# Kernel tuning notes

Hardware: AMD Instinct MI355X
Metric: run time of the kernel (lower is better)

The kernel has to match this reference:

```python
import jax, jax.numpy as jnp
import numpy as np

N = 50000       # population nodes
E = 1_600_000   # edges per edge type
F_IN = 2000     # flattened individual-graph embedding (100*20)
D = 20          # hidden channels per TransformerConv head (heads=1)
NEG_SLOPE = 0.01
BN_EPS = 1e-5


def setup_inputs() -> dict:
    key = jax.random.key(0)
    ks = jax.random.split(key, 24)
    features = jax.random.normal(ks[0], (N, F_IN), jnp.float32)
    same_index = jax.random.randint(ks[1], (2, E), 0, N, dtype=jnp.int64)
    diff_index = jax.random.randint(ks[2], (2, E), 0, N, dtype=jnp.int64)
    s0 = 1.0 / np.sqrt(F_IN)
    s1 = 1.0 / np.sqrt(D)
    # layer 0 conv params, stacked over the 2 edge types (same, diff)
    W0q = jax.random.normal(ks[3], (2, F_IN, D), jnp.float32) * s0
    W0k = jax.random.normal(ks[4], (2, F_IN, D), jnp.float32) * s0
    W0v = jax.random.normal(ks[5], (2, F_IN, D), jnp.float32) * s0
    W0s = jax.random.normal(ks[6], (2, F_IN, D), jnp.float32) * s0
    b0q = jnp.zeros((2, D)); b0k = jnp.zeros((2, D))
    b0v = jnp.zeros((2, D)); b0s = jnp.zeros((2, D))
    # layers 1..3 conv params: [layer, edge_type, D, D]
    Wq = jax.random.normal(ks[7], (3, 2, D, D), jnp.float32) * s1
    Wk = jax.random.normal(ks[8], (3, 2, D, D), jnp.float32) * s1
    Wv = jax.random.normal(ks[9], (3, 2, D, D), jnp.float32) * s1
    Ws = jax.random.normal(ks[10], (3, 2, D, D), jnp.float32) * s1
    bq = jnp.zeros((3, 2, D)); bk = jnp.zeros((3, 2, D))
    bv = jnp.zeros((3, 2, D)); bs = jnp.zeros((3, 2, D))
    w1 = jnp.full((4,), 0.8, jnp.float32)
    w2 = jnp.full((4,), 0.2, jnp.float32)
    bn_gamma = jnp.ones((4, D), jnp.float32)
    bn_beta = jnp.zeros((4, D), jnp.float32)
    Wout = jax.random.normal(ks[11], (4 * D, 2), jnp.float32) / np.sqrt(4 * D)
    bout = jnp.zeros((2,), jnp.float32)
    return dict(features=features, same_index=same_index, diff_index=diff_index,
                W0q=W0q, b0q=b0q, W0k=W0k, b0k=b0k, W0v=W0v, b0v=b0v, W0s=W0s, b0s=b0s,
                Wq=Wq, bq=bq, Wk=Wk, bk=bk, Wv=Wv, bv=bv, Ws=Ws, bs=bs,
                w1=w1, w2=w2, bn_gamma=bn_gamma, bn_beta=bn_beta, Wout=Wout, bout=bout)


def _tconv(x, edge_index, Wq, bq, Wk, bk, Wv, bv, Ws, bs):
    """PyG TransformerConv, heads=1, concat=True, root_weight=True, no edge_attr."""
    src, dst = edge_index[0], edge_index[1]
    q = x @ Wq + bq   # [N, D]
    k = x @ Wk + bk
    v = x @ Wv + bv
    logits = jnp.einsum('ed,ed->e', q[dst], k[src]) / jnp.sqrt(jnp.float32(D))  # [E]
    m = jax.ops.segment_max(logits, dst, num_segments=N)
    m = jnp.where(jnp.isfinite(m), m, jnp.float32(0.0))  # nodes with no in-edges
    e = jnp.exp(logits - m[dst])
    z = jax.ops.segment_sum(e, dst, num_segments=N)
    alpha = e / (z[dst] + 1e-16)  # PyG softmax epsilon
    agg = jax.ops.segment_sum(alpha[:, None] * v[src], dst, num_segments=N)  # [N, D]
    return agg + x @ Ws + bs  # skip (root) connection


def _bn(x, gamma, beta):
    mu = x.mean(axis=0)
    var = x.var(axis=0)
    return (x - mu) * jax.lax.rsqrt(var + BN_EPS) * gamma + beta


def reference(features, same_index, diff_index,
              W0q, b0q, W0k, b0k, W0v, b0v, W0s, b0s,
              Wq, bq, Wk, bk, Wv, bv, Ws, bs,
              w1, w2, bn_gamma, bn_beta, Wout, bout):
    x = features
    fcs = []
    for l in range(4):
        if l == 0:
            p_same = (W0q[0], b0q[0], W0k[0], b0k[0], W0v[0], b0v[0], W0s[0], b0s[0])
            p_diff = (W0q[1], b0q[1], W0k[1], b0k[1], W0v[1], b0v[1], W0s[1], b0s[1])
        else:
            i = l - 1
            p_same = (Wq[i, 0], bq[i, 0], Wk[i, 0], bk[i, 0], Wv[i, 0], bv[i, 0], Ws[i, 0], bs[i, 0])
            p_diff = (Wq[i, 1], bq[i, 1], Wk[i, 1], bk[i, 1], Wv[i, 1], bv[i, 1], Ws[i, 1], bs[i, 1])
        x1 = _tconv(x, same_index, *p_same)
        x2 = _tconv(x, diff_index, *p_diff)
        t = w1[l] + w2[l]
        x = (w1[l] / t) * x1 + (w2[l] / t) * x2
        x = _bn(x, bn_gamma[l], bn_beta[l])
        x = jax.nn.leaky_relu(x, NEG_SLOPE)
        fcs.append(x)
    fc = jnp.concatenate(fcs, axis=-1)  # [N, 80]
    return fc @ Wout + bout  # [N, 2]
```

## Files before the change

### kernel.cpp

```cpp
#include <hip/hip_runtime.h>
#include <math.h>

#define N_NODES 50000
#define E_EDGES 1600000
#define F_IN    2000
#define D       20
#define NCOL    160
#define KPAD    2016

#define INV_SQRT_D 0.22360679774997896f

typedef __bf16 bf16x8 __attribute__((ext_vector_type(8)));
typedef __bf16 bf16x4 __attribute__((ext_vector_type(4)));
typedef float  f32x4  __attribute__((ext_vector_type(4)));

__global__ void pack_kernel(
    const float* __restrict__ W0q, const float* __restrict__ W0k,
    const float* __restrict__ W0v, const float* __restrict__ W0s,
    const float* __restrict__ b0q, const float* __restrict__ b0k,
    const float* __restrict__ b0v, const float* __restrict__ b0s,
    const float* __restrict__ Wq,  const float* __restrict__ Wk,
    const float* __restrict__ Wv,  const float* __restrict__ Ws_,
    const float* __restrict__ bq,  const float* __restrict__ bk,
    const float* __restrict__ bv,  const float* __restrict__ bs_,
    __bf16* __restrict__ B0, float* __restrict__ bias0,
    float* __restrict__ WL, float* __restrict__ biasL,
    float* __restrict__ bn, int* __restrict__ deg)
{
  long idx = (long)blockIdx.x * blockDim.x + threadIdx.x;
  if (idx < (long)NCOL*KPAD) {
    int col = (int)(idx / KPAD), k = (int)(idx % KPAD);
    int et = col / 80, r = col % 80, mat = r / 20, d = r % 20;
    const float* w = (mat==0)?W0q:(mat==1)?W0s:(mat==2)?W0k:W0v;
    float v = (k < F_IN) ? w[((size_t)et*F_IN + k)*D + d] : 0.f;
    B0[idx] = (__bf16)v;
    return;
  }
  idx -= (long)NCOL*KPAD;
  if (idx < 160) {
    int col = (int)idx;
    int et = col / 80, r = col % 80, mat = r / 20, d = r % 20;
    const float* b = (mat==0)?b0q:(mat==1)?b0s:(mat==2)?b0k:b0v;
    bias0[col] = b[et*D + d];
    return;
  }
  idx -= 160;
  if (idx < 9600) {
    int l = (int)(idx / 3200), rem = (int)(idx % 3200);
    int k = rem / NCOL, col = rem % NCOL;
    int et = col / 80, r = col % 80, mat = r / 20, d = r % 20;
    const float* w = (mat==0)?Wq:(mat==1)?Ws_:(mat==2)?Wk:Wv;
    WL[idx] = w[(((size_t)l*2 + et)*D + k)*D + d];
    return;
  }
  idx -= 9600;
  if (idx < 480) {
    int l = (int)(idx / NCOL), col = (int)(idx % NCOL);
    int et = col / 80, r = col % 80, mat = r / 20, d = r % 20;
    const float* b = (mat==0)?bq:(mat==1)?bs_:(mat==2)?bk:bv;
    biasL[idx] = b[(l*2 + et)*D + d];
    return;
  }
  idx -= 480;
  if (idx < 320) { bn[idx] = 0.f; return; }
  idx -= 320;
  if (idx < 2*N_NODES) { deg[idx] = 0; return; }
}

__global__ void hist_kernel(const int* __restrict__ same, const int* __restrict__ diff,
                            int* __restrict__ deg)
{
  long i = (long)blockIdx.x * blockDim.x + threadIdx.x;
  if (i >= 2L*E_EDGES) return;
  int et = (i >= E_EDGES) ? 1 : 0;
  long e = i - (long)et*E_EDGES;
  const int* ix = et ? diff : same;
  int dst = ix[E_EDGES + e];
  atomicAdd(&deg[(size_t)et*N_NODES + dst], 1);
}

__global__ void scan_kernel(const int* __restrict__ deg,
                            int* __restrict__ rowptr0, int* __restrict__ rowptr1,
                            int* __restrict__ next0, int* __restrict__ next1)
{
  const int et = blockIdx.x;
  const int* dg = deg + (size_t)et*N_NODES;
  int* rp = et ? rowptr1 : rowptr0;
  int* np = et ? next1 : next0;
  __shared__ int part[1024];
  const int t = threadIdx.x;
  const int per = (N_NODES + 1023) / 1024;
  const int b = t * per;
  const int e = (b + per < N_NODES) ? (b + per) : N_NODES;
  int s = 0;
  for (int i = b; i < e; i++) s += dg[i];
  part[t] = s;
  __syncthreads();
  for (int o = 1; o < 1024; o <<= 1) {
    int v = (t >= o) ? part[t-o] : 0;
    __syncthreads();
    part[t] += v;
    __syncthreads();
  }
  int run = (t == 0) ? 0 : part[t-1];
  for (int i = b; i < e; i++) {
    rp[i] = run; np[i] = run;
    run += dg[i];
  }
  if (t == 0) rp[N_NODES] = part[1023];
}

#define SC_EPT 16
#define SC_CHUNK (256*SC_EPT)
__global__ void scatter_kernel(const int* __restrict__ same, const int* __restrict__ diff,
                               int* __restrict__ next0, int* __restrict__ next1,
                               int* __restrict__ adj0, int* __restrict__ adj1)
{
  const int part  = blockIdx.x & 7;
  const int chunk = blockIdx.x >> 3;
  const int lo = part * (N_NODES/8);
  const int hi = lo + (N_NODES/8);
  const long i0 = (long)chunk * SC_CHUNK + threadIdx.x;
#pragma unroll
  for (int it = 0; it < SC_EPT; ++it) {
    long i = i0 + (long)it*256;
    if (i >= 2L*E_EDGES) break;
    int et = (i >= E_EDGES) ? 1 : 0;
    long e = i - (long)et*E_EDGES;
    const int* ix = et ? diff : same;
    int dst = ix[E_EDGES + e];
    if (dst >= lo && dst < hi) {
      int src = ix[e];
      int* np  = et ? next1 : next0;
      int* adj = et ? adj1  : adj0;
      int pos = atomicAdd(&np[dst], 1);
      adj[pos] = src;
    }
  }
}

__launch_bounds__(512)
__global__ void gemm0_mfma(const float* __restrict__ A,
                           const __bf16* __restrict__ Bt,
                           const float* __restrict__ bias,
                           __bf16* __restrict__ C)
{
  __shared__ __bf16 as[128*32];
  const int t    = threadIdx.x;
  const int lane = t & 63;
  const int wid  = t >> 6;
  const int wr   = wid >> 1;
  const int wc   = wid & 1;
  const int rb0  = blockIdx.x * 128;

  const int srow = t >> 2;
  const int skc  = (t & 3) * 8;
  const int arow = rb0 + srow;
  const float* aptr = A + (size_t)arow * F_IN;

  const int lrow = lane & 15;
  const int lkb  = (lane >> 4) * 8;

  f32x4 acc[2][5];
#pragma unroll
  for (int i = 0; i < 2; i++)
#pragma unroll
    for (int j = 0; j < 5; j++) acc[i][j] = (f32x4){0.f,0.f,0.f,0.f};

  float4 p0, p1;
  auto loadA = [&](int k0) {
    int k = k0 + skc;
    if (arow < N_NODES) {
      if (k + 8 <= F_IN) {
        p0 = *(const float4*)(aptr + k);
        p1 = *(const float4*)(aptr + k + 4);
      } else {
        float tmp[8];
#pragma unroll
        for (int i = 0; i < 8; i++) tmp[i] = (k + i < F_IN) ? aptr[k + i] : 0.f;
        p0 = make_float4(tmp[0],tmp[1],tmp[2],tmp[3]);
        p1 = make_float4(tmp[4],tmp[5],tmp[6],tmp[7]);
      }
    } else {
      p0 = make_float4(0,0,0,0); p1 = p0;
    }
  };

  loadA(0);
  for (int s = 0; s < 63; s++) {
    bf16x8 h;
    h[0]=(__bf16)p0.x; h[1]=(__bf16)p0.y; h[2]=(__bf16)p0.z; h[3]=(__bf16)p0.w;
    h[4]=(__bf16)p1.x; h[5]=(__bf16)p1.y; h[6]=(__bf16)p1.z; h[7]=(__bf16)p1.w;
    *(bf16x8*)&as[srow*32 + skc] = h;
    __syncthreads();
    if (s + 1 < 63) loadA((s + 1) * 32);

    bf16x8 af[2];
#pragma unroll
    for (int rf = 0; rf < 2; rf++)
      af[rf] = *(bf16x8*)&as[(wr*32 + rf*16 + lrow)*32 + lkb];
    bf16x8 bfr[5];
#pragma unroll
    for (int cf = 0; cf < 5; cf++)
      bfr[cf] = *(const bf16x8*)(Bt + (size_t)(wc*80 + cf*16 + lrow)*KPAD + s*32 + lkb);
#pragma unroll
    for (int rf = 0; rf < 2; rf++)
#pragma unroll
      for (int cf = 0; cf < 5; cf++)
        acc[rf][cf] = __builtin_amdgcn_mfma_f32_16x16x32_bf16(af[rf], bfr[cf], acc[rf][cf], 0, 0, 0);
    __syncthreads();
  }

#pragma unroll
  for (int rf = 0; rf < 2; rf++) {
#pragma unroll
    for (int cf = 0; cf < 5; cf++) {
      int col = wc*80 + cf*16 + lrow;
      float bv = bias[col];
#pragma unroll
      for (int j = 0; j < 4; j++) {
        int r = rb0 + wr*32 + rf*16 + (lane >> 4)*4 + j;
        if (r < N_NODES) C[(size_t)r*NCOL + col] = (__bf16)(acc[rf][cf][j] + bv);
      }
    }
  }
}

__launch_bounds__(256)
__global__ void proj_small_kernel(const float* __restrict__ x, const float* __restrict__ W,
                                  const float* __restrict__ bias, __bf16* __restrict__ C)
{
  __shared__ float ws[20*160];
  __shared__ float xs[16*20];
  const int t = threadIdx.x;
  const int n0 = blockIdx.x * 16;
#pragma unroll
  for (int i = 0; i < 13; i++) {
    int idx = t + i*256;
    if (idx < 3200) ws[idx] = W[idx];
  }
#pragma unroll
  for (int i = 0; i < 2; i++) {
    int idx = t + i*256;
    if (idx < 320) {
      int nl = idx / 20, k = idx % 20;
      int n = n0 + nl;
      xs[idx] = (n < N_NODES) ? x[(size_t)n*D + k] : 0.f;
    }
  }
  __syncthreads();
#pragma unroll
  for (int i = 0; i < 10; i++) {
    int idx = t + i*256;
    int nl = idx / NCOL, col = idx % NCOL;
    int n = n0 + nl;
    if (n < N_NODES) {
      float acc = bias[col];
#pragma unroll
      for (int k = 0; k < 20; k++) acc += xs[nl*20 + k] * ws[k*NCOL + col];
      C[(size_t)n*NCOL + col] = (__bf16)acc;
    }
  }
}

__launch_bounds__(256)
__global__ void attn_fused(const int* __restrict__ rp0, const int* __restrict__ adj0,
                           const int* __restrict__ rp1, const int* __restrict__ adj1,
                           const __bf16* __restrict__ proj,
                           const float* __restrict__ w1, const float* __restrict__ w2, int l,
                           float* __restrict__ xpre, float* __restrict__ bn)
{
  __shared__ float ls[40];
  const int t  = threadIdx.x;
  const int sl = t & 15;
  const int node = blockIdx.x*16 + (t >> 4);
  const bool valid = node < N_NODES;
  if (t < 40) ls[t] = 0.f;
  __syncthreads();

  const float wa = w1[l], wb = w2[l];
  const float cw[2] = { wa/(wa+wb), wb/(wa+wb) };
  float xacc[20];

#pragma unroll
  for (int et = 0; et < 2; et++) {
    float m = -INFINITY, z = 0.f;
    float S[20];
#pragma unroll
    for (int d = 0; d < 20; d++) S[d] = 0.f;

    const __bf16* rq = proj + (size_t)(valid ? node : 0)*NCOL + et*80;

    if (valid) {
      float qf[20];
      {
        bf16x8 q0 = *(const bf16x8*)(rq);
        bf16x8 q1 = *(const bf16x8*)(rq + 8);
        bf16x4 q2 = *(const bf16x4*)(rq + 16);
#pragma unroll
        for (int i = 0; i < 8; i++) { qf[i] = (float)q0[i]; qf[8+i] = (float)q1[i]; }
#pragma unroll
        for (int i = 0; i < 4; i++) qf[16+i] = (float)q2[i];
      }
      const int* rowptr = et ? rp1 : rp0;
      const int* adj    = et ? adj1 : adj0;
      const int beg = rowptr[node], end = rowptr[node+1];

      int i = beg + sl;
      for (; i + 16 < end; i += 32) {
        const int s0 = adj[i], s1 = adj[i+16];
        const __bf16* kva = proj + (size_t)s0*NCOL + et*80 + 40;
        const __bf16* kvb = proj + (size_t)s1*NCOL + et*80 + 40;
        bf16x8 a0 = *(const bf16x8*)(kva);
        bf16x8 a1 = *(const bf16x8*)(kva + 8);
        bf16x8 a2 = *(const bf16x8*)(kva + 16);
        bf16x8 a3 = *(const bf16x8*)(kva + 24);
        bf16x8 a4 = *(const bf16x8*)(kva + 32);
        bf16x8 b0 = *(const bf16x8*)(kvb);
        bf16x8 b1 = *(const bf16x8*)(kvb + 8);
        bf16x8 b2 = *(const bf16x8*)(kvb + 16);
        bf16x8 b3 = *(const bf16x8*)(kvb + 24);
        bf16x8 b4 = *(const bf16x8*)(kvb + 32);

        float d0 = 0.f, d1 = 0.f;
#pragma unroll
        for (int j = 0; j < 8; j++) { d0 += qf[j]*(float)a0[j];     d1 += qf[j]*(float)b0[j]; }
#pragma unroll
        for (int j = 0; j < 8; j++) { d0 += qf[8+j]*(float)a1[j];   d1 += qf[8+j]*(float)b1[j]; }
#pragma unroll
        for (int j = 0; j < 4; j++) { d0 += qf[16+j]*(float)a2[j];  d1 += qf[16+j]*(float)b2[j]; }
        d0 *= INV_SQRT_D; d1 *= INV_SQRT_D;

        float nm = fmaxf(fmaxf(m, d0), d1);
        float a  = __expf(m - nm);
        float w0 = __expf(d0 - nm);
        float w1v= __expf(d1 - nm);
        z = z*a + w0 + w1v;
#pragma unroll
        for (int d = 0; d < 4; d++) S[d]    = S[d]*a    + w0*(float)a2[4+d] + w1v*(float)b2[4+d];
#pragma unroll
        for (int d = 0; d < 8; d++) S[4+d]  = S[4+d]*a  + w0*(float)a3[d]   + w1v*(float)b3[d];
#pragma unroll
        for (int d = 0; d < 8; d++) S[12+d] = S[12+d]*a + w0*(float)a4[d]   + w1v*(float)b4[d];
        m = nm;
      }
      for (; i < end; i += 16) {
        const int s0 = adj[i];
        const __bf16* kva = proj + (size_t)s0*NCOL + et*80 + 40;
        bf16x8 a0 = *(const bf16x8*)(kva);
        bf16x8 a1 = *(const bf16x8*)(kva + 8);
        bf16x8 a2 = *(const bf16x8*)(kva + 16);
        bf16x8 a3 = *(const bf16x8*)(kva + 24);
        bf16x8 a4 = *(const bf16x8*)(kva + 32);
        float d0 = 0.f;
#pragma unroll
        for (int j = 0; j < 8; j++) d0 += qf[j]*(float)a0[j];
#pragma unroll
        for (int j = 0; j < 8; j++) d0 += qf[8+j]*(float)a1[j];
#pragma unroll
        for (int j = 0; j < 4; j++) d0 += qf[16+j]*(float)a2[j];
        d0 *= INV_SQRT_D;
        float nm = fmaxf(m, d0);
        float a  = __expf(m - nm);
        float w0 = __expf(d0 - nm);
        z = z*a + w0;
#pragma unroll
        for (int d = 0; d < 4; d++) S[d]    = S[d]*a    + w0*(float)a2[4+d];
#pragma unroll
        for (int d = 0; d < 8; d++) S[4+d]  = S[4+d]*a  + w0*(float)a3[d];
#pragma unroll
        for (int d = 0; d < 8; d++) S[12+d] = S[12+d]*a + w0*(float)a4[d];
        m = nm;
      }
    }

#pragma unroll
    for (int o = 8; o >= 1; o >>= 1) {
      float m2 = __shfl_xor(m, o, 64);
      float z2 = __shfl_xor(z, o, 64);
      float nm = fmaxf(m, m2);
      float a  = __expf(fminf(m  - nm, 0.f));
      float b  = __expf(fminf(m2 - nm, 0.f));
      z = z*a + z2*b;
#pragma unroll
      for (int d = 0; d < 20; d++) {
        float s2 = __shfl_xor(S[d], o, 64);
        S[d] = S[d]*a + s2*b;
      }
      m = nm;
    }

    if (valid && sl == 0) {
      const float inv = 1.f / (z + 1e-16f);
      const __bf16* sp = rq + 20;
      float sv[20];
      {
        bf16x4 s0 = *(const bf16x4*)(sp);
        bf16x8 s1 = *(const bf16x8*)(sp + 4);
        bf16x8 s2 = *(const bf16x8*)(sp + 12);
#pragma unroll
        for (int i = 0; i < 4; i++) sv[i] = (float)s0[i];
#pragma unroll
        for (int i = 0; i < 8; i++) { sv[4+i] = (float)s1[i]; sv[12+i] = (float)s2[i]; }
      }
      const float c = cw[et];
#pragma unroll
      for (int d = 0; d < 20; d++) {
        float val = c * (S[d]*inv + sv[d]);
        xacc[d] = (et == 0) ? val : (xacc[d] + val);
      }
    }
  }

  if (valid && sl == 0) {
    float* xo = xpre + (size_t)node*D;
#pragma unroll
    for (int j = 0; j < 5; j++) {
      float4 o4 = make_float4(xacc[4*j], xacc[4*j+1], xacc[4*j+2], xacc[4*j+3]);
      *(float4*)(xo + 4*j) = o4;
    }
#pragma unroll
    for (int d = 0; d < 20; d++) {
      atomicAdd(&ls[d], xacc[d]);
      atomicAdd(&ls[20+d], xacc[d]*xacc[d]);
    }
  }
  __syncthreads();
  if (t < 40) atomicAdd(&bn[t], ls[t]);
}

__global__ void bnapply_kernel(const float* __restrict__ xpre, const float* __restrict__ bn,
                               const float* __restrict__ gamma, const float* __restrict__ beta,
                               int l, float* __restrict__ out)
{
  const int i = blockIdx.x*256 + threadIdx.x;
  if (i >= N_NODES*D) return;
  const int d = i % D;
  const float mu  = bn[d] * (1.f/N_NODES);
  const float var = bn[20+d] * (1.f/N_NODES) - mu*mu;
  const float rs  = rsqrtf(var + 1e-5f);
  float v = (xpre[i] - mu) * rs * gamma[l*D+d] + beta[l*D+d];
  out[i] = (v > 0.f) ? v : 0.01f*v;
}

__global__ void final_kernel(const float* __restrict__ fcs, const float* __restrict__ Wout,
                             const float* __restrict__ bout, float* __restrict__ out)
{
  const int n = blockIdx.x*256 + threadIdx.x;
  if (n >= N_NODES) return;
  float a0 = bout[0], a1 = bout[1];
#pragma unroll
  for (int l = 0; l < 4; l++) {
    const float* base = fcs + (size_t)l*N_NODES*D + (size_t)n*D;
#pragma unroll
    for (int d = 0; d < D; d++) {
      float v = base[d];
      a0 += v * Wout[(l*D+d)*2 + 0];
      a1 += v * Wout[(l*D+d)*2 + 1];
    }
  }
  out[n*2+0] = a0;
  out[n*2+1] = a1;
}

extern "C" void kernel_launch(void* const* d_in, const int* in_sizes, int n_in,
                              void* d_out, int out_size, void* d_ws, size_t ws_size,
                              hipStream_t stream)
{
  const float* feat = (const float*)d_in[0];
  const int*   same = (const int*)d_in[1];
  const int*   diff = (const int*)d_in[2];
  const float* W0q = (const float*)d_in[3];
  const float* b0q = (const float*)d_in[4];
  const float* W0k = (const float*)d_in[5];
  const float* b0k = (const float*)d_in[6];
  const float* W0v = (const float*)d_in[7];
  const float* b0v = (const float*)d_in[8];
  const float* W0s = (const float*)d_in[9];
  const float* b0s = (const float*)d_in[10];
  const float* Wq  = (const float*)d_in[11];
  const float* bq  = (const float*)d_in[12];
  const float* Wk  = (const float*)d_in[13];
  const float* bk  = (const float*)d_in[14];
  const float* Wv  = (const float*)d_in[15];
  const float* bv  = (const float*)d_in[16];
  const float* Ws_ = (const float*)d_in[17];
  const float* bs_ = (const float*)d_in[18];
  const float* w1  = (const float*)d_in[19];
  const float* w2  = (const float*)d_in[20];
  const float* gamma = (const float*)d_in[21];
  const float* beta  = (const float*)d_in[22];
  const float* Wout  = (const float*)d_in[23];
  const float* bout  = (const float*)d_in[24];

  float* wsf  = (float*)d_ws;
  __bf16*  PROJ  = (__bf16*)wsf;
  float*   XPRE  = wsf + 6000000;
  float*   FCS   = wsf + 7000000;
  __bf16*  B0bf  = (__bf16*)(wsf + 11000000);
  float*   BIAS0 = wsf + 11161280;
  float*   WL    = wsf + 11161440;
  float*   BIASL = wsf + 11171040;
  float*   BN    = wsf + 11171520;
  int*     ib    = (int*)(wsf + 11171840);
  int* DEG  = ib;
  int* RP0  = ib + 100000;
  int* RP1  = ib + 150004;
  int* NX0  = ib + 200008;
  int* NX1  = ib + 250008;
  int* ADJ0 = ib + 300008;
  int* ADJ1 = ib + 1900008;

  const int packN = NCOL*KPAD + 160 + 9600 + 480 + 320 + 2*N_NODES;
  pack_kernel<<<(packN + 255)/256, 256, 0, stream>>>(
      W0q, W0k, W0v, W0s, b0q, b0k, b0v, b0s,
      Wq, Wk, Wv, Ws_, bq, bk, bv, bs_,
      B0bf, BIAS0, WL, BIASL, BN, DEG);

  hist_kernel<<<(2*E_EDGES + 255)/256, 256, 0, stream>>>(same, diff, DEG);
  scan_kernel<<<2, 1024, 0, stream>>>(DEG, RP0, RP1, NX0, NX1);
  {
    const long nchunk = (2L*E_EDGES + SC_CHUNK - 1) / SC_CHUNK;
    scatter_kernel<<<(int)(nchunk*8), 256, 0, stream>>>(same, diff, NX0, NX1, ADJ0, ADJ1);
  }

  for (int l = 0; l < 4; l++) {
    if (l == 0)
      gemm0_mfma<<<(N_NODES + 127)/128, 512, 0, stream>>>(feat, B0bf, BIAS0, PROJ);
    else
      proj_small_kernel<<<(N_NODES + 15)/16, 256, 0, stream>>>(
          FCS + (size_t)(l-1)*N_NODES*D, WL + (size_t)(l-1)*3200, BIASL + (size_t)(l-1)*160, PROJ);

    attn_fused<<<(N_NODES + 15)/16, 256, 0, stream>>>(
        RP0, ADJ0, RP1, ADJ1, PROJ, w1, w2, l, XPRE, BN + l*80);

    bnapply_kernel<<<(N_NODES*D + 255)/256, 256, 0, stream>>>(
        XPRE, BN + l*80, gamma, beta, l, FCS + (size_t)l*N_NODES*D);
  }

  final_kernel<<<(N_NODES + 255)/256, 256, 0, stream>>>(FCS, Wout, bout, (float*)d_out);
}
```

Baseline: 1.099 ms.

## Fold BN apply into consumers, split edge types per group, drop online max

Removes the separate batch-norm-apply kernel. The normalize and leaky-ReLU steps are folded into the next layer's small projection load and into the final output kernel, so only pre-BN activations are stored, one buffer per layer. The attention kernel now gives each edge type its own 16-lane group, doubling the number of groups per node, and combines the two results through shared memory. The online-softmax running max is replaced by a plain exp clamped at 80, which removes the rescale multiplies and one exp per step. This relies on attention scores staying small enough that the unshifted exponentials cannot overflow.

Result: slower. 1.141 ms (+3.8%).

```diff
diff --git a/kernel.cpp b/kernel.cpp
--- a/kernel.cpp
+++ b/kernel.cpp
@@ -227,11 +227,14 @@
 }
 
 __launch_bounds__(256)
-__global__ void proj_small_kernel(const float* __restrict__ x, const float* __restrict__ W,
-                                  const float* __restrict__ bias, __bf16* __restrict__ C)
+__global__ void proj_small_kernel(const float* __restrict__ xp, const float* __restrict__ bnl,
+                                  const float* __restrict__ gam, const float* __restrict__ bet,
+                                  const float* __restrict__ W, const float* __restrict__ bias,
+                                  __bf16* __restrict__ C)
 {
   __shared__ float ws[20*160];
   __shared__ float xs[16*20];
+  __shared__ float Ac[20], Bc[20];
   const int t = threadIdx.x;
   const int n0 = blockIdx.x * 16;
 #pragma unroll
@@ -239,13 +242,22 @@
     int idx = t + i*256;
     if (idx < 3200) ws[idx] = W[idx];
   }
+  if (t < 20) {
+    float mu  = bnl[t] * (1.f/N_NODES);
+    float var = bnl[20+t] * (1.f/N_NODES) - mu*mu;
+    float a = rsqrtf(var + 1e-5f) * gam[t];
+    Ac[t] = a; Bc[t] = bet[t] - mu*a;
+  }
+  __syncthreads();
 #pragma unroll
   for (int i = 0; i < 2; i++) {
     int idx = t + i*256;
     if (idx < 320) {
       int nl = idx / 20, k = idx % 20;
       int n = n0 + nl;
-      xs[idx] = (n < N_NODES) ? x[(size_t)n*D + k] : 0.f;
+      float x = (n < N_NODES) ? xp[(size_t)n*D + k] : 0.f;
+      float y = x*Ac[k] + Bc[k];
+      xs[idx] = (y > 0.f) ? y : 0.01f*y;
     }
   }
   __syncthreads();
@@ -270,193 +282,159 @@
                            const float* __restrict__ w1, const float* __restrict__ w2, int l,
                            float* __restrict__ xpre, float* __restrict__ bn)
 {
+  __shared__ float outs[16][20];
   __shared__ float ls[40];
   const int t  = threadIdx.x;
+  const int g  = t >> 4;
   const int sl = t & 15;
-  const int node = blockIdx.x*16 + (t >> 4);
+  const int node = blockIdx.x*8 + (g >> 1);
+  const int et   = g & 1;
   const bool valid = node < N_NODES;
   if (t < 40) ls[t] = 0.f;
+
+  float z = 0.f;
+  float S[20];
+#pragma unroll
+  for (int d = 0; d < 20; d++) S[d] = 0.f;
+
+  const __bf16* rq = proj + (size_t)(valid ? node : 0)*NCOL + et*80;
+
+  if (valid) {
+    float qf[20];
+    {
+      bf16x8 q0 = *(const bf16x8*)(rq);
+      bf16x8 q1 = *(const bf16x8*)(rq + 8);
+      bf16x4 q2 = *(const bf16x4*)(rq + 16);
+#pragma unroll
+      for (int i = 0; i < 8; i++) { qf[i] = (float)q0[i]; qf[8+i] = (float)q1[i]; }
+#pragma unroll
+      for (int i = 0; i < 4; i++) qf[16+i] = (float)q2[i];
+    }
+    const int* rowptr = et ? rp1 : rp0;
+    const int* adj    = et ? adj1 : adj0;
+    const int beg = rowptr[node], end = rowptr[node+1];
+
+    int i = beg + sl;
+    for (; i + 16 < end; i += 32) {
+      const int s0 = adj[i], s1 = adj[i+16];
+      const __bf16* kva = proj + (size_t)s0*NCOL + et*80 + 40;
+      const __bf16* kvb = proj + (size_t)s1*NCOL + et*80 + 40;
+      bf16x8 a0 = *(const bf16x8*)(kva);
+      bf16x8 a1 = *(const bf16x8*)(kva + 8);
+      bf16x8 a2 = *(const bf16x8*)(kva + 16);
+      bf16x8 a3 = *(const bf16x8*)(kva + 24);
+      bf16x8 a4 = *(const bf16x8*)(kva + 32);
+      bf16x8 b0 = *(const bf16x8*)(kvb);
+      bf16x8 b1 = *(const bf16x8*)(kvb + 8);
+      bf16x8 b2 = *(const bf16x8*)(kvb + 16);
+      bf16x8 b3 = *(const bf16x8*)(kvb + 24);
+      bf16x8 b4 = *(const bf16x8*)(kvb + 32);
+
+      float d0 = 0.f, d1 = 0.f;
+#pragma unroll
+      for (int j = 0; j < 8; j++) { d0 += qf[j]*(float)a0[j];     d1 += qf[j]*(float)b0[j]; }
+#pragma unroll
+      for (int j = 0; j < 8; j++) { d0 += qf[8+j]*(float)a1[j];   d1 += qf[8+j]*(float)b1[j]; }
+#pragma unroll
+      for (int j = 0; j < 4; j++) { d0 += qf[16+j]*(float)a2[j];  d1 += qf[16+j]*(float)b2[j]; }
+      const float w0 = __expf(fminf(d0*INV_SQRT_D, 80.f));
+      const float w1v= __expf(fminf(d1*INV_SQRT_D, 80.f));
+      z += w0 + w1v;
+#pragma unroll
+      for (int d = 0; d < 4; d++) S[d]    += w0*(float)a2[4+d] + w1v*(float)b2[4+d];
+#pragma unroll
+      for (int d = 0; d < 8; d++) S[4+d]  += w0*(float)a3[d]   + w1v*(float)b3[d];
+#pragma unroll
+      for (int d = 0; d < 8; d++) S[12+d] += w0*(float)a4[d]   + w1v*(float)b4[d];
+    }
+    if (i < end) {
+      const int s0 = adj[i];
+      const __bf16* kva = proj + (size_t)s0*NCOL + et*80 + 40;
+      bf16x8 a0 = *(const bf16x8*)(kva);
+      bf16x8 a1 = *(const bf16x8*)(kva + 8);
+      bf16x8 a2 = *(const bf16x8*)(kva + 16);
+      bf16x8 a3 = *(const bf16x8*)(kva + 24);
+      bf16x8 a4 = *(const bf16x8*)(kva + 32);
+      float d0 = 0.f;
+#pragma unroll
+      for (int j = 0; j < 8; j++) d0 += qf[j]*(float)a0[j];
+#pragma unroll
+      for (int j = 0; j < 8; j++) d0 += qf[8+j]*(float)a1[j];
+#pragma unroll
+      for (int j = 0; j < 4; j++) d0 += qf[16+j]*(float)a2[j];
+      const float w0 = __expf(fminf(d0*INV_SQRT_D, 80.f));
+      z += w0;
+#pragma unroll
+      for (int d = 0; d < 4; d++) S[d]    += w0*(float)a2[4+d];
+#pragma unroll
+      for (int d = 0; d < 8; d++) S[4+d]  += w0*(float)a3[d];
+#pragma unroll
+      for (int d = 0; d < 8; d++) S[12+d] += w0*(float)a4[d];
+    }
+  }
+
+#pragma unroll
+  for (int o = 8; o >= 1; o >>= 1) {
+    z += __shfl_xor(z, o, 64);
+#pragma unroll
+    for (int d = 0; d < 20; d++) S[d] += __shfl_xor(S[d], o, 64);
+  }
+
+  const float inv = (z > 0.f) ? 1.f/z : 0.f;
+  if (valid) {
+#pragma unroll
+    for (int d = sl; d < 20; d += 16)
+      outs[g][d] = S[d]*inv + (float)rq[20 + d];
+  }
   __syncthreads();
 
-  const float wa = w1[l], wb = w2[l];
-  const float cw[2] = { wa/(wa+wb), wb/(wa+wb) };
-  float xacc[20];
-
-#pragma unroll
-  for (int et = 0; et < 2; et++) {
-    float m = -INFINITY, z = 0.f;
-    float S[20];
-#pragma unroll
-    for (int d = 0; d < 20; d++) S[d] = 0.f;
-
-    const __bf16* rq = proj + (size_t)(valid ? node : 0)*NCOL + et*80;
-
-    if (valid) {
-      float qf[20];
-      {
-        bf16x8 q0 = *(const bf16x8*)(rq);
-        bf16x8 q1 = *(const bf16x8*)(rq + 8);
-        bf16x4 q2 = *(const bf16x4*)(rq + 16);
-#pragma unroll
-        for (int i = 0; i < 8; i++) { qf[i] = (float)q0[i]; qf[8+i] = (float)q1[i]; }
-#pragma unroll
-        for (int i = 0; i < 4; i++) qf[16+i] = (float)q2[i];
-      }
-      const int* rowptr = et ? rp1 : rp0;
-      const int* adj    = et ? adj1 : adj0;
-      const int beg = rowptr[node], end = rowptr[node+1];
-
-      int i = beg + sl;
-      for (; i + 16 < end; i += 32) {
-        const int s0 = adj[i], s1 = adj[i+16];
-        const __bf16* kva = proj + (size_t)s0*NCOL + et*80 + 40;
-        const __bf16* kvb = proj + (size_t)s1*NCOL + et*80 + 40;
-        bf16x8 a0 = *(const bf16x8*)(kva);
-        bf16x8 a1 = *(const bf16x8*)(kva + 8);
-        bf16x8 a2 = *(const bf16x8*)(kva + 16);
-        bf16x8 a3 = *(const bf16x8*)(kva + 24);
-        bf16x8 a4 = *(const bf16x8*)(kva + 32);
-        bf16x8 b0 = *(const bf16x8*)(kvb);
-        bf16x8 b1 = *(const bf16x8*)(kvb + 8);
-        bf16x8 b2 = *(const bf16x8*)(kvb + 16);
-        bf16x8 b3 = *(const bf16x8*)(kvb + 24);
-        bf16x8 b4 = *(const bf16x8*)(kvb + 32);
-
-        float d0 = 0.f, d1 = 0.f;
-#pragma unroll
-        for (int j = 0; j < 8; j++) { d0 += qf[j]*(float)a0[j];     d1 += qf[j]*(float)b0[j]; }
-#pragma unroll
-        for (int j = 0; j < 8; j++) { d0 += qf[8+j]*(float)a1[j];   d1 += qf[8+j]*(float)b1[j]; }
-#pragma unroll
-        for (int j = 0; j < 4; j++) { d0 += qf[16+j]*(float)a2[j];  d1 += qf[16+j]*(float)b2[j]; }
-        d0 *= INV_SQRT_D; d1 *= INV_SQRT_D;
-
-        float nm = fmaxf(fmaxf(m, d0), d1);
-        float a  = __expf(m - nm);
-        float w0 = __expf(d0 - nm);
-        float w1v= __expf(d1 - nm);
-        z = z*a + w0 + w1v;
-#pragma unroll
-        for (int d = 0; d < 4; d++) S[d]    = S[d]*a    + w0*(float)a2[4+d] + w1v*(float)b2[4+d];
-#pragma unroll
-        for (int d = 0; d < 8; d++) S[4+d]  = S[4+d]*a  + w0*(float)a3[d]   + w1v*(float)b3[d];
-#pragma unroll
-        for (int d = 0; d < 8; d++) S[12+d] = S[12+d]*a + w0*(float)a4[d]   + w1v*(float)b4[d];
-        m = nm;
-      }
-      for (; i < end; i += 16) {
-        const int s0 = adj[i];
-        const __bf16* kva = proj + (size_t)s0*NCOL + et*80 + 40;
-        bf16x8 a0 = *(const bf16x8*)(kva);
-        bf16x8 a1 = *(const bf16x8*)(kva + 8);
-        bf16x8 a2 = *(const bf16x8*)(kva + 16);
-        bf16x8 a3 = *(const bf16x8*)(kva + 24);
-        bf16x8 a4 = *(const bf16x8*)(kva + 32);
-        float d0 = 0.f;
-#pragma unroll
-        for (int j = 0; j < 8; j++) d0 += qf[j]*(float)a0[j];
-#pragma unroll
-        for (int j = 0; j < 8; j++) d0 += qf[8+j]*(float)a1[j];
-#pragma unroll
-        for (int j = 0; j < 4; j++) d0 += qf[16+j]*(float)a2[j];
-        d0 *= INV_SQRT_D;
-        float nm = fmaxf(m, d0);
-        float a  = __expf(m - nm);
-        float w0 = __expf(d0 - nm);
-        z = z*a + w0;
-#pragma unroll
-        for (int d = 0; d < 4; d++) S[d]    = S[d]*a    + w0*(float)a2[4+d];
-#pragma unroll
-        for (int d = 0; d < 8; d++) S[4+d]  = S[4+d]*a  + w0*(float)a3[d];
-#pragma unroll
-        for (int d = 0; d < 8; d++) S[12+d] = S[12+d]*a + w0*(float)a4[d];
-        m = nm;
-      }
-    }
-
-#pragma unroll
-    for (int o = 8; o >= 1; o >>= 1) {
-      float m2 = __shfl_xor(m, o, 64);
-      float z2 = __shfl_xor(z, o, 64);
-      float nm = fmaxf(m, m2);
-      float a  = __expf(fminf(m  - nm, 0.f));
-      float b  = __expf(fminf(m2 - nm, 0.f));
-      z = z*a + z2*b;
-#pragma unroll
-      for (int d = 0; d < 20; d++) {
-        float s2 = __shfl_xor(S[d], o, 64);
-        S[d] = S[d]*a + s2*b;
-      }
-      m = nm;
-    }
-
-    if (valid && sl == 0) {
-      const float inv = 1.f / (z + 1e-16f);
-      const __bf16* sp = rq + 20;
-      float sv[20];
-      {
-        bf16x4 s0 = *(const bf16x4*)(sp);
-        bf16x8 s1 = *(const bf16x8*)(sp + 4);
-        bf16x8 s2 = *(const bf16x8*)(sp + 12);
-#pragma unroll
-        for (int i = 0; i < 4; i++) sv[i] = (float)s0[i];
-#pragma unroll
-        for (int i = 0; i < 8; i++) { sv[4+i] = (float)s1[i]; sv[12+i] = (float)s2[i]; }
-      }
-      const float c = cw[et];
-#pragma unroll
-      for (int d = 0; d < 20; d++) {
-        float val = c * (S[d]*inv + sv[d]);
-        xacc[d] = (et == 0) ? val : (xacc[d] + val);
-      }
-    }
-  }
-
-  if (valid && sl == 0) {
-    float* xo = xpre + (size_t)node*D;
-#pragma unroll
-    for (int j = 0; j < 5; j++) {
-      float4 o4 = make_float4(xacc[4*j], xacc[4*j+1], xacc[4*j+2], xacc[4*j+3]);
-      *(float4*)(xo + 4*j) = o4;
-    }
-#pragma unroll
-    for (int d = 0; d < 20; d++) {
-      atomicAdd(&ls[d], xacc[d]);
-      atomicAdd(&ls[20+d], xacc[d]*xacc[d]);
+  if (valid && et == 0) {
+    const float wa = w1[l], wb = w2[l];
+    const float cw0 = wa/(wa+wb), cw1 = wb/(wa+wb);
+#pragma unroll
+    for (int d = sl; d < 20; d += 16) {
+      float x = cw0*outs[g][d] + cw1*outs[g|1][d];
+      xpre[(size_t)node*D + d] = x;
+      atomicAdd(&ls[d], x);
+      atomicAdd(&ls[20+d], x*x);
     }
   }
   __syncthreads();
   if (t < 40) atomicAdd(&bn[t], ls[t]);
 }
 
-__global__ void bnapply_kernel(const float* __restrict__ xpre, const float* __restrict__ bn,
-                               const float* __restrict__ gamma, const float* __restrict__ beta,
-                               int l, float* __restrict__ out)
-{
-  const int i = blockIdx.x*256 + threadIdx.x;
-  if (i >= N_NODES*D) return;
-  const int d = i % D;
-  const float mu  = bn[d] * (1.f/N_NODES);
-  const float var = bn[20+d] * (1.f/N_NODES) - mu*mu;
-  const float rs  = rsqrtf(var + 1e-5f);
-  float v = (xpre[i] - mu) * rs * gamma[l*D+d] + beta[l*D+d];
-  out[i] = (v > 0.f) ? v : 0.01f*v;
-}
-
-__global__ void final_kernel(const float* __restrict__ fcs, const float* __restrict__ Wout,
-                             const float* __restrict__ bout, float* __restrict__ out)
-{
-  const int n = blockIdx.x*256 + threadIdx.x;
+__launch_bounds__(256)
+__global__ void final_kernel(const float* __restrict__ xpre4, const float* __restrict__ bn,
+                             const float* __restrict__ gam, const float* __restrict__ bet,
+                             const float* __restrict__ Wout, const float* __restrict__ bout,
+                             float* __restrict__ out)
+{
+  __shared__ float Ac[80], Bc[80], wlds[160];
+  const int t = threadIdx.x;
+  if (t < 80) {
+    int l = t / 20, d = t % 20;
+    const float* b = bn + l*80;
+    float mu  = b[d] * (1.f/N_NODES);
+    float var = b[20+d] * (1.f/N_NODES) - mu*mu;
+    float a = rsqrtf(var + 1e-5f) * gam[t];
+    Ac[t] = a; Bc[t] = bet[t] - mu*a;
+  }
+  if (t < 160) wlds[t] = Wout[t];
+  __syncthreads();
+
+  const int n = blockIdx.x*256 + t;
   if (n >= N_NODES) return;
   float a0 = bout[0], a1 = bout[1];
 #pragma unroll
   for (int l = 0; l < 4; l++) {
-    const float* base = fcs + (size_t)l*N_NODES*D + (size_t)n*D;
+    const float* base = xpre4 + (size_t)l*N_NODES*D + (size_t)n*D;
 #pragma unroll
     for (int d = 0; d < D; d++) {
-      float v = base[d];
-      a0 += v * Wout[(l*D+d)*2 + 0];
-      a1 += v * Wout[(l*D+d)*2 + 1];
+      int idx = l*20 + d;
+      float y = base[d]*Ac[idx] + Bc[idx];
+      y = (y > 0.f) ? y : 0.01f*y;
+      a0 += y * wlds[idx*2 + 0];
+      a1 += y * wlds[idx*2 + 1];
     }
   }
   out[n*2+0] = a0;
@@ -495,14 +473,13 @@
 
   float* wsf  = (float*)d_ws;
   __bf16*  PROJ  = (__bf16*)wsf;
-  float*   XPRE  = wsf + 6000000;
-  float*   FCS   = wsf + 7000000;
-  __bf16*  B0bf  = (__bf16*)(wsf + 11000000);
-  float*   BIAS0 = wsf + 11161280;
-  float*   WL    = wsf + 11161440;
-  float*   BIASL = wsf + 11171040;
-  float*   BN    = wsf + 11171520;
-  int*     ib    = (int*)(wsf + 11171840);
+  float*   XPRE4 = wsf + 4000000;
+  __bf16*  B0bf  = (__bf16*)(wsf + 8000000);
+  float*   BIAS0 = wsf + 8161280;
+  float*   WL    = wsf + 8161440;
+  float*   BIASL = wsf + 8171040;
+  float*   BN    = wsf + 8171520;
+  int*     ib    = (int*)(wsf + 8171840);
   int* DEG  = ib;
   int* RP0  = ib + 100000;
   int* RP1  = ib + 150004;
@@ -529,14 +506,14 @@
       gemm0_mfma<<<(N_NODES + 127)/128, 512, 0, stream>>>(feat, B0bf, BIAS0, PROJ);
     else
       proj_small_kernel<<<(N_NODES + 15)/16, 256, 0, stream>>>(
-          FCS + (size_t)(l-1)*N_NODES*D, WL + (size_t)(l-1)*3200, BIASL + (size_t)(l-1)*160, PROJ);
-
-    attn_fused<<<(N_NODES + 15)/16, 256, 0, stream>>>(
-        RP0, ADJ0, RP1, ADJ1, PROJ, w1, w2, l, XPRE, BN + l*80);
-
-    bnapply_kernel<<<(N_NODES*D + 255)/256, 256, 0, stream>>>(
-        XPRE, BN + l*80, gamma, beta, l, FCS + (size_t)l*N_NODES*D);
-  }
-
-  final_kernel<<<(N_NODES + 255)/256, 256, 0, stream>>>(FCS, Wout, bout, (float*)d_out);
-}
+          XPRE4 + (size_t)(l-1)*N_NODES*D, BN + (l-1)*80,
+          gamma + (l-1)*D, beta + (l-1)*D,
+          WL + (size_t)(l-1)*3200, BIASL + (size_t)(l-1)*160, PROJ);
+
+    attn_fused<<<(N_NODES + 7)/8, 256, 0, stream>>>(
+        RP0, ADJ0, RP1, ADJ1, PROJ, w1, w2, l, XPRE4 + (size_t)l*N_NODES*D, BN + l*80);
+  }
+
+  final_kernel<<<(N_NODES + 255)/256, 256, 0, stream>>>(
+      XPRE4, BN, gamma, beta, Wout, bout, (float*)d_out);
+}
```
